# Performance work log

Measured on AMD Instinct MI355X. Metric: run time of the kernel, lower is better.

## Reference

```python
import jax, jax.numpy as jnp
import numpy as np

B, S, D, H = 2, 2048, 2048, 16
HD = D // H

def setup_inputs() -> dict:
    key = jax.random.key(0)
    ks = jax.random.split(key, 6)
    x = jax.random.normal(ks[0], (B, S, D), dtype=jnp.float32)
    # causal mask: 1 where attention allowed, 0 where masked
    mask = jnp.tril(jnp.ones((S, S), dtype=jnp.int32))[None, None, :, :]
    scale_w = 0.02
    W_qkv = jax.random.normal(ks[1], (D, 3 * D), dtype=jnp.float32) * scale_w
    b_qkv = jnp.zeros((3 * D,), dtype=jnp.float32)
    W_proj = jax.random.normal(ks[2], (D, D), dtype=jnp.float32) * scale_w
    b_proj = jnp.zeros((D,), dtype=jnp.float32)
    return {"x": x, "W_qkv": W_qkv, "b_qkv": b_qkv, "W_proj": W_proj, "b_proj": b_proj, "mask": mask}

def reference(x, W_qkv, b_qkv, W_proj, b_proj, mask):
    b, s, d = x.shape
    qkv = x @ W_qkv + b_qkv                       # [b,s,3d]
    qkv = qkv.reshape(b, s, 3, H, HD)
    q = jnp.transpose(qkv[:, :, 0], (0, 2, 1, 3))  # [b,h,s,hd]
    k = jnp.transpose(qkv[:, :, 1], (0, 2, 1, 3))
    v = jnp.transpose(qkv[:, :, 2], (0, 2, 1, 3))
    scale = HD ** -0.5
    attn = jnp.einsum('bhqd,bhkd->bhqk', q, k) * scale
    attn = jnp.where(mask == 0, -jnp.inf, attn)
    attn = jax.nn.softmax(attn, axis=-1)
    # dropout is identity in eval mode
    out = jnp.einsum('bhqk,bhkd->bhqd', attn, v)   # [b,h,s,hd]
    out = jnp.transpose(out, (0, 2, 1, 3)).reshape(b, s, d)
    return out @ W_proj + b_proj
```

## Files before the change

### kernel.cpp

```cpp
#include <hip/hip_runtime.h>
#include <hip/hip_bf16.h>
#include <math.h>

#define BATCH 2
#define SEQ   2048
#define DIM   2048
#define NH    16
#define HD    128
#define QKV_N (3 * DIM)
#define TOKENS (BATCH * SEQ)

typedef __attribute__((ext_vector_type(8))) short bf16x8;
typedef __attribute__((ext_vector_type(4))) float f32x4;

typedef __attribute__((address_space(1))) const void* as1cv;
typedef __attribute__((address_space(3))) void* as3v;

__device__ __forceinline__ short f2bf(float x) {
    unsigned u = __float_as_uint(x);
    u += 0x7fffu + ((u >> 16) & 1u);
    return (short)(u >> 16);
}

__device__ __forceinline__ void gload16(const short* g, short* lds) {
    __builtin_amdgcn_global_load_lds((as1cv)g, (as3v)lds, 16, 0, 0);
}

__global__ __launch_bounds__(256)
void f32_to_bf16_kernel(const float* __restrict__ in, short* __restrict__ out) {
    const size_t i = ((size_t)blockIdx.x * 256 + threadIdx.x) * 8;
    const float4 a = *reinterpret_cast<const float4*>(in + i);
    const float4 b = *reinterpret_cast<const float4*>(in + i + 4);
    bf16x8 v;
    v[0] = f2bf(a.x); v[1] = f2bf(a.y); v[2] = f2bf(a.z); v[3] = f2bf(a.w);
    v[4] = f2bf(b.x); v[5] = f2bf(b.y); v[6] = f2bf(b.z); v[7] = f2bf(b.w);
    *reinterpret_cast<bf16x8*>(out + i) = v;
}

__global__ __launch_bounds__(256)
void transpose_f32_to_bf16(const float* __restrict__ W, short* __restrict__ Wt,
                           int K, int N) {
    __shared__ float t[64][65];
    const int tid = threadIdx.x;
    const int n0 = blockIdx.x * 64;
    const int k0 = blockIdx.y * 64;
    const int tc = tid & 63, tr = tid >> 6;
    #pragma unroll
    for (int i = 0; i < 16; ++i)
        t[tr + i * 4][tc] = W[(size_t)(k0 + tr + i * 4) * N + n0 + tc];
    __syncthreads();
    #pragma unroll
    for (int i = 0; i < 16; ++i)
        Wt[(size_t)(n0 + tr + i * 4) * K + k0 + tc] = f2bf(t[tc][tr + i * 4]);
}

template <bool BF16OUT>
__global__ __launch_bounds__(256, 2)
void gemm_mfma_kernel(const short* __restrict__ A, const short* __restrict__ Bt,
                      const float* __restrict__ bias, void* __restrict__ Cv,
                      int M, int N, int K, int nM) {
    __shared__ short A_lds[2][128 * 64];
    __shared__ short B_lds[2][128 * 64];

    const int tid  = threadIdx.x;
    const int lane = tid & 63;
    const int w    = tid >> 6;
    const int lr   = lane & 15;
    const int lhi  = lane >> 4;
    const int wr   = w >> 1;
    const int wc   = w & 1;

    const int nwg  = gridDim.x;
    const int cpx  = nwg >> 3;
    const int orig = blockIdx.x;
    const int wg   = (orig & 7) * cpx + (orig >> 3);
    const int bm   = (wg % nM) * 128;
    const int bn   = (wg / nM) * 128;

    const int srow   = tid >> 3;
    const int schunk = (tid & 7) ^ (srow & 7);
    const short* gA = A  + (size_t)(bm + srow) * K + schunk * 8;
    const short* gB = Bt + (size_t)(bn + srow) * K + schunk * 8;

    const int nt = K >> 6;

    auto STAGE = [&](int t, int buf) {
        const int ko = t * 64;
        short* la = &A_lds[buf][w * 512];
        short* lb = &B_lds[buf][w * 512];
        #pragma unroll
        for (int i = 0; i < 4; ++i)
            gload16(gA + (size_t)(i * 32) * K + ko, la + i * 2048);
        #pragma unroll
        for (int i = 0; i < 4; ++i)
            gload16(gB + (size_t)(i * 32) * K + ko, lb + i * 2048);
    };

    f32x4 acc[4][4] = {};

    STAGE(0, 0);
    STAGE(1, 1);
    asm volatile("s_waitcnt vmcnt(8)" ::: "memory");
    __builtin_amdgcn_s_barrier();

    int cur = 0;
    for (int t = 0; t < nt; ++t, cur ^= 1) {
        bf16x8 af[2][4], bfr[2][4];
        const short* Ab = &A_lds[cur][0];
        const short* Bb = &B_lds[cur][0];
        #pragma unroll
        for (int ks = 0; ks < 2; ++ks) {
            const int cb = ks * 4 + lhi;
            #pragma unroll
            for (int mi = 0; mi < 4; ++mi) {
                const int r = wr * 64 + mi * 16 + lr;
                af[ks][mi] = *reinterpret_cast<const bf16x8*>(
                    &Ab[r * 64 + ((cb ^ (r & 7)) << 3)]);
            }
            #pragma unroll
            for (int ni = 0; ni < 4; ++ni) {
                const int c = wc * 64 + ni * 16 + lr;
                bfr[ks][ni] = *reinterpret_cast<const bf16x8*>(
                    &Bb[c * 64 + ((cb ^ (c & 7)) << 3)]);
            }
        }
        asm volatile("s_waitcnt lgkmcnt(0)" ::: "memory");
        __builtin_amdgcn_sched_barrier(0);
        __builtin_amdgcn_s_barrier();
        __builtin_amdgcn_sched_barrier(0);

        if (t + 2 < nt) STAGE(t + 2, cur);

        __builtin_amdgcn_s_setprio(1);
        #pragma unroll
        for (int ks = 0; ks < 2; ++ks)
            #pragma unroll
            for (int mi = 0; mi < 4; ++mi)
                #pragma unroll
                for (int ni = 0; ni < 4; ++ni)
                    acc[mi][ni] = __builtin_amdgcn_mfma_f32_16x16x32_bf16(
                        af[ks][mi], bfr[ks][ni], acc[mi][ni], 0, 0, 0);
        __builtin_amdgcn_s_setprio(0);
        __builtin_amdgcn_sched_barrier(0);

        if (t + 2 < nt) {
            asm volatile("s_waitcnt vmcnt(8)" ::: "memory");
            __builtin_amdgcn_s_barrier();
        } else if (t + 1 < nt) {
            asm volatile("s_waitcnt vmcnt(0)" ::: "memory");
            __builtin_amdgcn_s_barrier();
        }
    }

    #pragma unroll
    for (int mi = 0; mi < 4; ++mi) {
        #pragma unroll
        for (int j = 0; j < 4; ++j) {
            const int r = bm + wr * 64 + mi * 16 + lhi * 4 + j;
            #pragma unroll
            for (int ni = 0; ni < 4; ++ni) {
                const int c = bn + wc * 64 + ni * 16 + lr;
                const float v = acc[mi][ni][j] + bias[c];
                if (BF16OUT) ((short*)Cv)[(size_t)r * N + c] = f2bf(v);
                else         ((float*)Cv)[(size_t)r * N + c] = v;
            }
        }
    }
}

__device__ __forceinline__ int swz8(int row) {
    return ((row ^ (row >> 2)) & 7) << 3;
}

__global__ __launch_bounds__(256)
void attn_mfma_kernel(const short* __restrict__ qkv, short* __restrict__ out) {
    __shared__ short K_lds[64 * 128];
    __shared__ short VT_lds[128 * 64];
    __shared__ short P_lds[4 * 16 * 64];

    const int tid  = threadIdx.x;
    const int lane = tid & 63;
    const int w    = tid >> 6;

    const int z    = blockIdx.x;
    const int qblk = (SEQ / 64 - 1) - (z >> 5);
    const int bh   = z & 31;
    const int h    = bh & 15;
    const int b    = bh >> 4;

    const int q0 = qblk * 64;
    const size_t tokbase = (size_t)b * SEQ * QKV_N;

    const int lr  = lane & 15;
    const int lhi = lane >> 4;
    const int qrow = q0 + w * 16 + lr;
    const short* qrowp = qkv + tokbase + (size_t)qrow * QKV_N + h * HD;
    bf16x8 qfrag[4];
    #pragma unroll
    for (int ks = 0; ks < 4; ++ks)
        qfrag[ks] = *reinterpret_cast<const bf16x8*>(qrowp + ks * 32 + lhi * 8);

    f32x4 o[8] = {};
    float m[4], l[4];
    #pragma unroll
    for (int j = 0; j < 4; ++j) { m[j] = -3.0e38f; l[j] = 0.f; }

    const float scale = 0.08838834764831845f;
    const int wq0 = q0 + w * 16;
    const int ntiles = qblk + 1;

    for (int t = 0; t < ntiles; ++t) {
        {
            const int r  = tid >> 2;
            const int q4 = tid & 3;
            const size_t rowb = tokbase + (size_t)(t * 64 + r) * QKV_N + h * HD + q4 * 32;
            const short* krow = qkv + rowb + DIM;
            const short* vrow = qkv + rowb + 2 * DIM;
            short* kdst = &K_lds[r * 128];
            #pragma unroll
            for (int cc = 0; cc < 4; ++cc) {
                bf16x8 kv8 = *reinterpret_cast<const bf16x8*>(krow + cc * 8);
                *reinterpret_cast<bf16x8*>(kdst + ((q4 * 32 + cc * 8) ^ swz8(r))) = kv8;
            }
            #pragma unroll
            for (int cc = 0; cc < 4; ++cc) {
                bf16x8 vv8 = *reinterpret_cast<const bf16x8*>(vrow + cc * 8);
                #pragma unroll
                for (int j = 0; j < 8; ++j) {
                    const int d = q4 * 32 + cc * 8 + j;
                    VT_lds[d * 64 + (r ^ swz8(d))] = vv8[j];
                }
            }
        }
        __syncthreads();

        f32x4 s[4] = {};
        #pragma unroll
        for (int ks = 0; ks < 4; ++ks) {
            #pragma unroll
            for (int cg = 0; cg < 4; ++cg) {
                const int row = cg * 16 + lr;
                const bf16x8 kf = *reinterpret_cast<const bf16x8*>(
                    &K_lds[row * 128 + ((ks * 32 + lhi * 8) ^ swz8(row))]);
                s[cg] = __builtin_amdgcn_mfma_f32_16x16x32_bf16(qfrag[ks], kf, s[cg], 0, 0, 0);
            }
        }

        #pragma unroll
        for (int j = 0; j < 4; ++j) {
            const int qg = wq0 + lhi * 4 + j;
            float mx = -3.0e38f;
            #pragma unroll
            for (int cg = 0; cg < 4; ++cg) {
                const int kvg = t * 64 + cg * 16 + lr;
                float sv = s[cg][j] * scale;
                if (kvg > qg) sv = -3.0e38f;
                s[cg][j] = sv;
                mx = fmaxf(mx, sv);
            }
            #pragma unroll
            for (int off = 1; off < 16; off <<= 1) mx = fmaxf(mx, __shfl_xor(mx, off));
            const float mnew = fmaxf(m[j], mx);
            const float corr = __expf(m[j] - mnew);
            m[j] = mnew;
            float rsum = 0.f;
            #pragma unroll
            for (int cg = 0; cg < 4; ++cg) {
                const float e = __expf(s[cg][j] - mnew);
                s[cg][j] = e;
                rsum += e;
            }
            #pragma unroll
            for (int off = 1; off < 16; off <<= 1) rsum += __shfl_xor(rsum, off);
            l[j] = l[j] * corr + rsum;
            #pragma unroll
            for (int cg = 0; cg < 8; ++cg) o[cg][j] *= corr;
        }

        short* pbase = &P_lds[w * 1024];
        #pragma unroll
        for (int cg = 0; cg < 4; ++cg) {
            #pragma unroll
            for (int j = 0; j < 4; ++j) {
                const int rw = lhi * 4 + j;
                const int c  = cg * 16 + lr;
                pbase[rw * 64 + (c ^ swz8(rw))] = f2bf(s[cg][j]);
            }
        }
        bf16x8 pa[2];
        #pragma unroll
        for (int ks = 0; ks < 2; ++ks)
            pa[ks] = *reinterpret_cast<const bf16x8*>(
                &pbase[lr * 64 + ((ks * 32 + lhi * 8) ^ swz8(lr))]);

        #pragma unroll
        for (int cg = 0; cg < 8; ++cg) {
            #pragma unroll
            for (int ks = 0; ks < 2; ++ks) {
                const int d = cg * 16 + lr;
                const bf16x8 vf = *reinterpret_cast<const bf16x8*>(
                    &VT_lds[d * 64 + ((ks * 32 + lhi * 8) ^ swz8(d))]);
                o[cg] = __builtin_amdgcn_mfma_f32_16x16x32_bf16(pa[ks], vf, o[cg], 0, 0, 0);
            }
        }
        __syncthreads();
    }

    #pragma unroll
    for (int j = 0; j < 4; ++j) {
        const float inv = 1.f / l[j];
        const int qg = q0 + w * 16 + lhi * 4 + j;
        short* op = out + (size_t)(b * SEQ + qg) * DIM + h * HD;
        #pragma unroll
        for (int cg = 0; cg < 8; ++cg)
            op[cg * 16 + lr] = f2bf(o[cg][j] * inv);
    }
}

extern "C" void kernel_launch(void* const* d_in, const int* in_sizes, int n_in,
                              void* d_out, int out_size, void* d_ws, size_t ws_size,
                              hipStream_t stream) {
    const float* x      = (const float*)d_in[0];
    const float* W_qkv  = (const float*)d_in[1];
    const float* b_qkv  = (const float*)d_in[2];
    const float* W_proj = (const float*)d_in[3];
    const float* b_proj = (const float*)d_in[4];

    float* out = (float*)d_out;

    short* qkv_bf  = (short*)d_ws;
    short* attn_bf = qkv_bf  + (size_t)TOKENS * QKV_N;
    short* x_bf    = attn_bf + (size_t)TOKENS * DIM;
    short* wqkv_t  = x_bf    + (size_t)TOKENS * DIM;
    short* wproj_t = wqkv_t  + (size_t)DIM * QKV_N;

    f32_to_bf16_kernel<<<TOKENS * DIM / (256 * 8), 256, 0, stream>>>(x, x_bf);
    {
        dim3 g(QKV_N / 64, DIM / 64);
        transpose_f32_to_bf16<<<g, 256, 0, stream>>>(W_qkv, wqkv_t, DIM, QKV_N);
    }
    {
        dim3 g(DIM / 64, DIM / 64);
        transpose_f32_to_bf16<<<g, 256, 0, stream>>>(W_proj, wproj_t, DIM, DIM);
    }

    {
        const int nM = TOKENS / 128, nN = QKV_N / 128;
        gemm_mfma_kernel<true><<<nM * nN, 256, 0, stream>>>(
            x_bf, wqkv_t, b_qkv, (void*)qkv_bf, TOKENS, QKV_N, DIM, nM);
    }
    attn_mfma_kernel<<<BATCH * NH * (SEQ / 64), 256, 0, stream>>>(qkv_bf, attn_bf);

    {
        const int nM = TOKENS / 128, nN = DIM / 128;
        gemm_mfma_kernel<false><<<nM * nN, 256, 0, stream>>>(
            attn_bf, wproj_t, b_proj, (void*)out, TOKENS, DIM, DIM, nM);
    }
}
```

Before: 284.5 us.

## Prescale Q, mask only diagonal tile, lazy softmax rescale, new V swizzle

The softmax scale is folded into the Q fragments at load time, which re-rounds Q to bf16. The causal mask is now applied only on the diagonal tile. The online-softmax rescale of the output and running sum is skipped unless the tile max exceeds the running max by more than a threshold (checked wave-wide), which cuts exp and multiply work per tile. A new XOR swizzle is used for the transposed V layout in LDS to reduce bank conflicts on the scattered writes. The extra Q rounding and the deferred rescale slightly change the numerics; the threshold keeps exp values bounded.

```diff
diff --git a/kernel.cpp b/kernel.cpp
--- a/kernel.cpp
+++ b/kernel.cpp
@@ -20,6 +20,10 @@
     unsigned u = __float_as_uint(x);
     u += 0x7fffu + ((u >> 16) & 1u);
     return (short)(u >> 16);
+}
+
+__device__ __forceinline__ float bf2f(short x) {
+    return __uint_as_float(((unsigned)(unsigned short)x) << 16);
 }
 
 __device__ __forceinline__ void gload16(const short* g, short* lds) {
@@ -171,6 +175,9 @@
 __device__ __forceinline__ int swz8(int row) {
     return ((row ^ (row >> 2)) & 7) << 3;
 }
+__device__ __forceinline__ int swzV(int d) {
+    return ((d ^ (d >> 2) ^ ((d >> 5) << 1)) & 7) << 3;
+}
 
 __global__ __launch_bounds__(256)
 void attn_mfma_kernel(const short* __restrict__ qkv, short* __restrict__ out) {
@@ -193,19 +200,25 @@
 
     const int lr  = lane & 15;
     const int lhi = lane >> 4;
+    const float scale = 0.08838834764831845f;
+
     const int qrow = q0 + w * 16 + lr;
     const short* qrowp = qkv + tokbase + (size_t)qrow * QKV_N + h * HD;
     bf16x8 qfrag[4];
     #pragma unroll
-    for (int ks = 0; ks < 4; ++ks)
-        qfrag[ks] = *reinterpret_cast<const bf16x8*>(qrowp + ks * 32 + lhi * 8);
+    for (int ks = 0; ks < 4; ++ks) {
+        bf16x8 v = *reinterpret_cast<const bf16x8*>(qrowp + ks * 32 + lhi * 8);
+        bf16x8 sv;
+        #pragma unroll
+        for (int e = 0; e < 8; ++e) sv[e] = f2bf(bf2f(v[e]) * scale);
+        qfrag[ks] = sv;
+    }
 
     f32x4 o[8] = {};
     float m[4], l[4];
     #pragma unroll
     for (int j = 0; j < 4; ++j) { m[j] = -3.0e38f; l[j] = 0.f; }
 
-    const float scale = 0.08838834764831845f;
     const int wq0 = q0 + w * 16;
     const int ntiles = qblk + 1;
 
@@ -228,7 +241,7 @@
                 #pragma unroll
                 for (int j = 0; j < 8; ++j) {
                     const int d = q4 * 32 + cc * 8 + j;
-                    VT_lds[d * 64 + (r ^ swz8(d))] = vv8[j];
+                    VT_lds[d * 64 + (r ^ swzV(d))] = vv8[j];
                 }
             }
         }
@@ -246,35 +259,38 @@
             }
         }
 
+        const bool diag = (t == qblk);
         #pragma unroll
         for (int j = 0; j < 4; ++j) {
-            const int qg = wq0 + lhi * 4 + j;
-            float mx = -3.0e38f;
+            if (diag) {
+                const int qg = wq0 + lhi * 4 + j;
+                #pragma unroll
+                for (int cg = 0; cg < 4; ++cg) {
+                    const int kvg = t * 64 + cg * 16 + lr;
+                    if (kvg > qg) s[cg][j] = -3.0e38f;
+                }
+            }
+            float pmax = fmaxf(fmaxf(s[0][j], s[1][j]), fmaxf(s[2][j], s[3][j]));
+            #pragma unroll
+            for (int off = 1; off < 16; off <<= 1) pmax = fmaxf(pmax, __shfl_xor(pmax, off));
+            if (!__all(pmax <= m[j] + 8.f)) {
+                const float mnew = fmaxf(m[j], pmax);
+                const float corr = __expf(m[j] - mnew);
+                m[j] = mnew;
+                l[j] *= corr;
+                #pragma unroll
+                for (int cg = 0; cg < 8; ++cg) o[cg][j] *= corr;
+            }
+            float rsum = 0.f;
             #pragma unroll
             for (int cg = 0; cg < 4; ++cg) {
-                const int kvg = t * 64 + cg * 16 + lr;
-                float sv = s[cg][j] * scale;
-                if (kvg > qg) sv = -3.0e38f;
-                s[cg][j] = sv;
-                mx = fmaxf(mx, sv);
-            }
-            #pragma unroll
-            for (int off = 1; off < 16; off <<= 1) mx = fmaxf(mx, __shfl_xor(mx, off));
-            const float mnew = fmaxf(m[j], mx);
-            const float corr = __expf(m[j] - mnew);
-            m[j] = mnew;
-            float rsum = 0.f;
-            #pragma unroll
-            for (int cg = 0; cg < 4; ++cg) {
-                const float e = __expf(s[cg][j] - mnew);
+                const float e = __expf(s[cg][j] - m[j]);
                 s[cg][j] = e;
                 rsum += e;
             }
             #pragma unroll
             for (int off = 1; off < 16; off <<= 1) rsum += __shfl_xor(rsum, off);
-            l[j] = l[j] * corr + rsum;
-            #pragma unroll
-            for (int cg = 0; cg < 8; ++cg) o[cg][j] *= corr;
+            l[j] += rsum;
         }
 
         short* pbase = &P_lds[w * 1024];
@@ -299,7 +315,7 @@
             for (int ks = 0; ks < 2; ++ks) {
                 const int d = cg * 16 + lr;
                 const bf16x8 vf = *reinterpret_cast<const bf16x8*>(
-                    &VT_lds[d * 64 + ((ks * 32 + lhi * 8) ^ swz8(d))]);
+                    &VT_lds[d * 64 + ((ks * 32 + lhi * 8) ^ swzV(d))]);
                 o[cg] = __builtin_amdgcn_mfma_f32_16x16x32_bf16(pa[ks], vf, o[cg], 0, 0, 0);
             }
         }
```

After: 368.4 us. 1.29x slower.
